# Performance work log

Measured on AMD Instinct MI355X. Metric: run time of the kernel, lower is better.

The kernel has to match this reference:

```python
import jax, jax.numpy as jnp
import numpy as np

B, H, M, D, MID, DV = 128, 8, 196, 128, 64, 128


def setup_inputs() -> dict:
    key0 = jax.random.key(0)
    ks = jax.random.split(key0, 12)
    query = jax.random.normal(ks[0], (B, H, D), dtype=jnp.float32)
    key = jax.random.normal(ks[1], (B, H, M, D), dtype=jnp.float32)
    att_mask = jax.random.randint(ks[2], (B, M), 0, 2).astype(jnp.float32)
    att_mask = att_mask.at[:, 0].set(1.0)  # guarantee each row has >=1 valid slot
    value1 = jax.random.normal(ks[3], (B, H, DV), dtype=jnp.float32)
    value2 = jax.random.normal(ks[4], (B, H, M, DV), dtype=jnp.float32)
    W_basic = jax.random.normal(ks[5], (D, MID), dtype=jnp.float32) * 0.05
    b_basic = jnp.zeros((MID,), dtype=jnp.float32)
    W_spatial = jax.random.normal(ks[6], (MID, 1), dtype=jnp.float32) * 0.05
    b_spatial = jnp.zeros((1,), dtype=jnp.float32)
    W_channel = jax.random.normal(ks[7], (MID, DV), dtype=jnp.float32) * 0.05
    b_channel = jnp.zeros((DV,), dtype=jnp.float32)
    return {
        'query': query, 'key': key, 'att_mask': att_mask,
        'value1': value1, 'value2': value2,
        'W_basic': W_basic, 'b_basic': b_basic,
        'W_spatial': W_spatial, 'b_spatial': b_spatial,
        'W_channel': W_channel, 'b_channel': b_channel,
    }


def reference(query, key, att_mask, value1, value2,
              W_basic, b_basic, W_spatial, b_spatial, W_channel, b_channel):
    # att_map: broadcast elementwise QK product  [B,H,M,D]
    att_map = query[..., None, :] * key
    # attention_basic: Linear + ReLU (Dropout is identity at eval)  [B,H,M,MID]
    h = jax.nn.relu(jnp.einsum('bhmd,de->bhme', att_map, W_basic) + b_basic)
    # masked mean-pool over regions  [B,H,MID]
    mask_ext = att_mask[:, None, :, None]  # [B,1,M,1]
    att_map_pool = jnp.sum(h * mask_ext, axis=-2) / jnp.sum(mask_ext, axis=-2)
    # spatial attention logits  [B,H,M]
    alpha_spatial = (jnp.einsum('bhme,eo->bhmo', h, W_spatial) + b_spatial)[..., 0]
    alpha_spatial = jnp.where(att_mask[:, None, :] == 0, -1e9, alpha_spatial)
    alpha_spatial = jax.nn.softmax(alpha_spatial, axis=-1)
    # weighted sum over regions  [B,H,DV]
    v2 = jnp.einsum('bhm,bhmv->bhv', alpha_spatial, value2)
    # channel gate  [B,H,DV]
    alpha_channel = jax.nn.sigmoid(jnp.einsum('bhe,ev->bhv', att_map_pool, W_channel) + b_channel)
    return value1 * v2 * alpha_channel
```

## Files before the change

kernel.cpp:

```cpp
#include <hip/hip_runtime.h>
#include <cstddef>

#define NBH  1024
#define Mm   196
#define Dd   128
#define MIDe 64
#define DVv  128
#define WQLD 136

typedef __attribute__((ext_vector_type(8))) short bf16x8;
typedef __attribute__((ext_vector_type(4))) float f32x4;

__device__ __forceinline__ short f2bf(float x) {
    union { float f; unsigned u; } v; v.f = x;
    return (short)((v.u + 0x7FFFu + ((v.u >> 16) & 1u)) >> 16);
}

__device__ __forceinline__ void gl_lds16(const void* g, void* l) {
    __builtin_amdgcn_global_load_lds(
        (const __attribute__((address_space(1))) unsigned int*)g,
        (__attribute__((address_space(3))) unsigned int*)l, 16, 0, 0);
}

__global__ __launch_bounds__(256, 2)
void scatt_fused(const float* __restrict__ query,
                 const float* __restrict__ key,
                 const float* __restrict__ att_mask,
                 const float* __restrict__ value1,
                 const float* __restrict__ value2,
                 const float* __restrict__ W_basic,
                 const float* __restrict__ b_basic,
                 const float* __restrict__ W_spatial,
                 const float* __restrict__ b_spatial,
                 const float* __restrict__ W_channel,
                 const float* __restrict__ b_channel,
                 float* __restrict__ out)
{
    __shared__ float4 kb[2][32][16];
    __shared__ short  wqT[MIDe][WQLD];
    __shared__ float  qS[Dd];
    __shared__ float  maskS[Mm];
    __shared__ float  poolS[MIDe];

    const int t    = threadIdx.x;
    const int lane = t & 63;
    const int w    = t >> 6;
    const int ln15 = lane & 15;
    const int q4   = lane >> 4;
    const int bh   = blockIdx.x;
    const int b    = bh >> 3;

    const char*  keyC  = (const char*)(key + (size_t)bh * Mm * Dd);
    const float* val2B = value2   + (size_t)bh * Mm * DVv;
    const float* qB    = query    + (size_t)bh * Dd;
    const float* maskB = att_mask + (size_t)b  * Mm;

    const int cell0 = w * 128 + lane;
    const int cell1 = cell0 + 64;
    const int r0 = cell0 & 15, d40 = cell0 >> 4;
    const int r1 = cell1 & 15, d41 = cell1 >> 4;
    const int so0  = r0 * 512 + d40 * 16;
    const int so1  = r1 * 512 + d41 * 16;
    const int soT0 = (r0 < 4 ? r0 : 3) * 512 + d40 * 16;
    const int soT1 = (r1 < 4 ? r1 : 3) * 512 + d41 * 16;
    const int colOff = w * 32 + 2 * ln15;

    gl_lds16(keyC + so0, (char*)kb + w * 2048);
    gl_lds16(keyC + so1, (char*)kb + w * 2048 + 1024);
    float2 vvA[4], vvB[4];
#pragma unroll
    for (int rr = 0; rr < 4; ++rr)
        vvA[rr] = *(const float2*)(val2B + (size_t)(q4 * 4 + rr) * DVv + colOff);

    if (t < 32) ((float4*)qS)[t] = ((const float4*)qB)[t];
    for (int i = t; i < Mm; i += 256) maskS[i] = maskB[i];
    __syncthreads();
    {
        const int e0 = lane;
        const int d0 = w * 32;
#pragma unroll
        for (int c = 0; c < 4; ++c) {
            short pk[8];
#pragma unroll
            for (int j = 0; j < 8; ++j) {
                const int d = d0 + c * 8 + j;
                pk[j] = f2bf(qS[d] * W_basic[d * MIDe + e0]);
            }
            *(bf16x8*)&wqT[e0][d0 + c * 8] = *(bf16x8*)pk;
        }
    }
    __syncthreads();

    float bbv[4], wspv[4];
#pragma unroll
    for (int nt = 0; nt < 4; ++nt) {
        bbv[nt]  = b_basic[nt * 16 + ln15];
        wspv[nt] = W_spatial[nt * 16 + ln15];
    }
    const float bsp = b_spatial[0];

    float poolAcc[4] = {0.f, 0.f, 0.f, 0.f};
    float m_run = -3.0e38f, l_run = 0.f;
    float2 av = make_float2(0.f, 0.f);

#define TILE_STEP(MT, PAR, VCUR, VNXT, PF)                                   \
    do {                                                                     \
        asm volatile("s_waitcnt vmcnt(4)" ::: "memory");                     \
        __builtin_amdgcn_s_barrier();                                        \
        __builtin_amdgcn_sched_barrier(0);                                   \
        if (PF) {                                                            \
            char* db = (char*)kb + ((PAR) ^ 1) * 8192;                       \
            const char* sb = keyC + (size_t)((MT) + 1) * 8192;               \
            if ((PF) == 1) {                                                 \
                gl_lds16(sb + so0, db + w * 2048);                           \
                gl_lds16(sb + so1, db + w * 2048 + 1024);                    \
            } else {                                                         \
                gl_lds16(sb + soT0, db + w * 2048);                          \
                gl_lds16(sb + soT1, db + w * 2048 + 1024);                   \
            }                                                                \
            __builtin_amdgcn_sched_barrier(0);                               \
            _Pragma("unroll")                                                \
            for (int rr = 0; rr < 4; ++rr) {                                 \
                int vrow = ((MT) + 1) * 16 + q4 * 4 + rr;                    \
                if ((PF) == 2) vrow = vrow < Mm ? vrow : (Mm - 1);           \
                VNXT[rr] =                                                   \
                    *(const float2*)(val2B + (size_t)vrow * DVv + colOff);   \
            }                                                                \
        }                                                                    \
        const char* kbB = (const char*)kb + (PAR) * 8192;                    \
        f32x4 acc[4] = {f32x4{0,0,0,0}, f32x4{0,0,0,0},                      \
                        f32x4{0,0,0,0}, f32x4{0,0,0,0}};                     \
        _Pragma("unroll")                                                    \
        for (int ks = 0; ks < 4; ++ks) {                                     \
            const int d4 = ks * 8 + q4 * 2;                                  \
            const float4 f0 = *(const float4*)(kbB + d4 * 256 + ln15 * 16);  \
            const float4 f1 =                                                \
                *(const float4*)(kbB + d4 * 256 + 256 + ln15 * 16);          \
            const bf16x8 af = { f2bf(f0.x), f2bf(f0.y), f2bf(f0.z),          \
                                f2bf(f0.w), f2bf(f1.x), f2bf(f1.y),          \
                                f2bf(f1.z), f2bf(f1.w) };                    \
            _Pragma("unroll")                                                \
            for (int nt = 0; nt < 4; ++nt) {                                 \
                const bf16x8 bk =                                            \
                    *(const bf16x8*)&wqT[nt * 16 + ln15][ks * 32 + q4 * 8];  \
                acc[nt] = __builtin_amdgcn_mfma_f32_16x16x32_bf16(           \
                              af, bk, acc[nt], 0, 0, 0);                     \
            }                                                                \
        }                                                                    \
        float sR[4];                                                         \
        _Pragma("unroll")                                                    \
        for (int rr = 0; rr < 4; ++rr) {                                     \
            const int m = (MT) * 16 + q4 * 4 + rr;                           \
            const bool valid = m < Mm;                                       \
            const float msk = valid ? maskS[m] : 0.f;                        \
            float srow = 0.f;                                                \
            _Pragma("unroll")                                                \
            for (int nt = 0; nt < 4; ++nt) {                                 \
                float hv = acc[nt][rr] + bbv[nt];                            \
                hv = hv > 0.f ? hv : 0.f;                                    \
                poolAcc[nt] = fmaf(hv, msk, poolAcc[nt]);                    \
                srow = fmaf(hv, wspv[nt], srow);                             \
            }                                                                \
            srow += __shfl_xor(srow, 1, 64);                                 \
            srow += __shfl_xor(srow, 2, 64);                                 \
            srow += __shfl_xor(srow, 4, 64);                                 \
            srow += __shfl_xor(srow, 8, 64);                                 \
            sR[rr] = valid ? (msk == 0.f ? -1.0e9f : srow + bsp) : -3.0e38f; \
        }                                                                    \
        float tm = fmaxf(fmaxf(sR[0], sR[1]), fmaxf(sR[2], sR[3]));          \
        tm = fmaxf(tm, __shfl_xor(tm, 16, 64));                              \
        tm = fmaxf(tm, __shfl_xor(tm, 32, 64));                              \
        const float newm = fmaxf(m_run, tm);                                 \
        const float sc = __expf(m_run - newm);                               \
        m_run = newm;                                                        \
        l_run *= sc; av.x *= sc; av.y *= sc;                                 \
        _Pragma("unroll")                                                    \
        for (int rr = 0; rr < 4; ++rr) {                                     \
            const float p = __expf(sR[rr] - newm);                           \
            l_run += p;                                                      \
            av.x = fmaf(p, VCUR[rr].x, av.x);                                \
            av.y = fmaf(p, VCUR[rr].y, av.y);                                \
        }                                                                    \
    } while (0)

    for (int mtp = 0; mtp < 5; ++mtp) {
        const int mt0 = 2 * mtp;
        TILE_STEP(mt0,     0, vvA, vvB, 1);
        TILE_STEP(mt0 + 1, 1, vvB, vvA, 1);
    }
    TILE_STEP(10, 0, vvA, vvB, 1);
    TILE_STEP(11, 1, vvB, vvA, 2);
    TILE_STEP(12, 0, vvA, vvB, 0);
#undef TILE_STEP

#pragma unroll
    for (int nt = 0; nt < 4; ++nt) {
        poolAcc[nt] += __shfl_xor(poolAcc[nt], 16, 64);
        poolAcc[nt] += __shfl_xor(poolAcc[nt], 32, 64);
    }
    l_run += __shfl_xor(l_run, 16, 64);
    l_run += __shfl_xor(l_run, 32, 64);
    av.x  += __shfl_xor(av.x, 16, 64);
    av.x  += __shfl_xor(av.x, 32, 64);
    av.y  += __shfl_xor(av.y, 16, 64);
    av.y  += __shfl_xor(av.y, 32, 64);

    float cnt = 0.f;
    for (int i = lane; i < Mm; i += 64) cnt += maskS[i];
#pragma unroll
    for (int off = 32; off > 0; off >>= 1) cnt += __shfl_xor(cnt, off, 64);

    if (w == 0 && lane < 16) {
#pragma unroll
        for (int nt = 0; nt < 4; ++nt)
            poolS[nt * 16 + lane] = poolAcc[nt] / cnt;
    }
    __syncthreads();

    const float v2x = av.x / l_run;
    const float v2y = av.y / l_run;

    float a0 = 0.f, a1 = 0.f;
#pragma unroll
    for (int i = 0; i < 16; ++i) {
        const int e = q4 * 16 + i;
        const float pe = poolS[e];
        const float2 wc = *(const float2*)(W_channel + (size_t)e * DVv + colOff);
        a0 = fmaf(pe, wc.x, a0);
        a1 = fmaf(pe, wc.y, a1);
    }
    a0 += __shfl_xor(a0, 16, 64); a0 += __shfl_xor(a0, 32, 64);
    a1 += __shfl_xor(a1, 16, 64); a1 += __shfl_xor(a1, 32, 64);

    if (q4 == 0) {
        const float2 bc = *(const float2*)(b_channel + colOff);
        const float ch0 = 1.f / (1.f + __expf(-(a0 + bc.x)));
        const float ch1 = 1.f / (1.f + __expf(-(a1 + bc.y)));
        const float2 v1 = *(const float2*)(value1 + (size_t)bh * DVv + colOff);
        float2 o;
        o.x = v1.x * v2x * ch0;
        o.y = v1.y * v2y * ch1;
        *(float2*)(out + (size_t)bh * DVv + colOff) = o;
    }
}

extern "C" void kernel_launch(void* const* d_in, const int* in_sizes, int n_in,
                              void* d_out, int out_size, void* d_ws, size_t ws_size,
                              hipStream_t stream) {
    const float* query     = (const float*)d_in[0];
    const float* key       = (const float*)d_in[1];
    const float* att_mask  = (const float*)d_in[2];
    const float* value1    = (const float*)d_in[3];
    const float* value2    = (const float*)d_in[4];
    const float* W_basic   = (const float*)d_in[5];
    const float* b_basic   = (const float*)d_in[6];
    const float* W_spatial = (const float*)d_in[7];
    const float* b_spatial = (const float*)d_in[8];
    const float* W_channel = (const float*)d_in[9];
    const float* b_channel = (const float*)d_in[10];
    float* out = (float*)d_out;

    scatt_fused<<<NBH, 256, 0, stream>>>(query, key, att_mask, value1, value2,
                                         W_basic, b_basic, W_spatial, b_spatial,
                                         W_channel, b_channel, out);
}
```

Measured before the change: 255.1 us.

## Deepen key/value prefetch to triple-buffered LDS with two-tile lookahead

Expands the key LDS buffer from two stages to three and prefetches tiles two steps ahead, with a third register set for value2 rows. Key fragments are now read from LDS and converted to bf16 before the next prefetch is issued, so the barrier protects the buffer being overwritten. The aim is to hide more global-load latency per tile. The cost is more LDS (another 8 KB) and more registers, which may reduce occupancy under the 2-blocks launch bound. The hand-set vmcnt wait counts must stay correct for this to be safe.

```diff
diff --git a/kernel.cpp b/kernel.cpp
--- a/kernel.cpp
+++ b/kernel.cpp
@@ -36,7 +36,7 @@
                  const float* __restrict__ b_channel,
                  float* __restrict__ out)
 {
-    __shared__ float4 kb[2][32][16];
+    __shared__ float4 kb[3][32][16];
     __shared__ short  wqT[MIDe][WQLD];
     __shared__ float  qS[Dd];
     __shared__ float  maskS[Mm];
@@ -67,7 +67,7 @@
 
     gl_lds16(keyC + so0, (char*)kb + w * 2048);
     gl_lds16(keyC + so1, (char*)kb + w * 2048 + 1024);
-    float2 vvA[4], vvB[4];
+    float2 vvA[4], vvB[4], vvC[4];
 #pragma unroll
     for (int rr = 0; rr < 4; ++rr)
         vvA[rr] = *(const float2*)(val2B + (size_t)(q4 * 4 + rr) * DVv + colOff);
@@ -91,6 +91,12 @@
     }
     __syncthreads();
 
+    gl_lds16(keyC + 8192 + so0, (char*)kb + 8192 + w * 2048);
+    gl_lds16(keyC + 8192 + so1, (char*)kb + 8192 + w * 2048 + 1024);
+#pragma unroll
+    for (int rr = 0; rr < 4; ++rr)
+        vvB[rr] = *(const float2*)(val2B + (size_t)(16 + q4 * 4 + rr) * DVv + colOff);
+
     float bbv[4], wspv[4];
 #pragma unroll
     for (int nt = 0; nt < 4; ++nt) {
@@ -103,14 +109,26 @@
     float m_run = -3.0e38f, l_run = 0.f;
     float2 av = make_float2(0.f, 0.f);
 
-#define TILE_STEP(MT, PAR, VCUR, VNXT, PF)                                   \
+#define TILE_STEP(MT, PAR, PNX, VCUR, VN2, PF, WAITASM)                      \
     do {                                                                     \
-        asm volatile("s_waitcnt vmcnt(4)" ::: "memory");                     \
+        asm volatile(WAITASM ::: "memory");                                  \
         __builtin_amdgcn_s_barrier();                                        \
         __builtin_amdgcn_sched_barrier(0);                                   \
+        const char* kbB = (const char*)kb + (PAR) * 8192;                    \
+        bf16x8 af[4];                                                        \
+        _Pragma("unroll")                                                    \
+        for (int ks = 0; ks < 4; ++ks) {                                     \
+            const int d4 = ks * 8 + q4 * 2;                                  \
+            const float4 f0 = *(const float4*)(kbB + d4 * 256 + ln15 * 16);  \
+            const float4 f1 =                                                \
+                *(const float4*)(kbB + d4 * 256 + 256 + ln15 * 16);          \
+            af[ks] = bf16x8{ f2bf(f0.x), f2bf(f0.y), f2bf(f0.z), f2bf(f0.w), \
+                             f2bf(f1.x), f2bf(f1.y), f2bf(f1.z), f2bf(f1.w)};\
+        }                                                                    \
+        __builtin_amdgcn_sched_barrier(0);                                   \
         if (PF) {                                                            \
-            char* db = (char*)kb + ((PAR) ^ 1) * 8192;                       \
-            const char* sb = keyC + (size_t)((MT) + 1) * 8192;               \
+            char* db = (char*)kb + (PNX) * 8192;                             \
+            const char* sb = keyC + (size_t)((MT) + 2) * 8192;               \
             if ((PF) == 1) {                                                 \
                 gl_lds16(sb + so0, db + w * 2048);                           \
                 gl_lds16(sb + so1, db + w * 2048 + 1024);                    \
@@ -118,33 +136,25 @@
                 gl_lds16(sb + soT0, db + w * 2048);                          \
                 gl_lds16(sb + soT1, db + w * 2048 + 1024);                   \
             }                                                                \
-            __builtin_amdgcn_sched_barrier(0);                               \
             _Pragma("unroll")                                                \
             for (int rr = 0; rr < 4; ++rr) {                                 \
-                int vrow = ((MT) + 1) * 16 + q4 * 4 + rr;                    \
+                int vrow = ((MT) + 2) * 16 + q4 * 4 + rr;                    \
                 if ((PF) == 2) vrow = vrow < Mm ? vrow : (Mm - 1);           \
-                VNXT[rr] =                                                   \
+                VN2[rr] =                                                    \
                     *(const float2*)(val2B + (size_t)vrow * DVv + colOff);   \
             }                                                                \
-        }                                                                    \
-        const char* kbB = (const char*)kb + (PAR) * 8192;                    \
+            __builtin_amdgcn_sched_barrier(0);                               \
+        }                                                                    \
         f32x4 acc[4] = {f32x4{0,0,0,0}, f32x4{0,0,0,0},                      \
                         f32x4{0,0,0,0}, f32x4{0,0,0,0}};                     \
         _Pragma("unroll")                                                    \
         for (int ks = 0; ks < 4; ++ks) {                                     \
-            const int d4 = ks * 8 + q4 * 2;                                  \
-            const float4 f0 = *(const float4*)(kbB + d4 * 256 + ln15 * 16);  \
-            const float4 f1 =                                                \
-                *(const float4*)(kbB + d4 * 256 + 256 + ln15 * 16);          \
-            const bf16x8 af = { f2bf(f0.x), f2bf(f0.y), f2bf(f0.z),          \
-                                f2bf(f0.w), f2bf(f1.x), f2bf(f1.y),          \
-                                f2bf(f1.z), f2bf(f1.w) };                    \
             _Pragma("unroll")                                                \
             for (int nt = 0; nt < 4; ++nt) {                                 \
                 const bf16x8 bk =                                            \
                     *(const bf16x8*)&wqT[nt * 16 + ln15][ks * 32 + q4 * 8];  \
                 acc[nt] = __builtin_amdgcn_mfma_f32_16x16x32_bf16(           \
-                              af, bk, acc[nt], 0, 0, 0);                     \
+                              af[ks], bk, acc[nt], 0, 0, 0);                 \
             }                                                                \
         }                                                                    \
         float sR[4];                                                         \
@@ -183,14 +193,16 @@
         }                                                                    \
     } while (0)
 
-    for (int mtp = 0; mtp < 5; ++mtp) {
-        const int mt0 = 2 * mtp;
-        TILE_STEP(mt0,     0, vvA, vvB, 1);
-        TILE_STEP(mt0 + 1, 1, vvB, vvA, 1);
-    }
-    TILE_STEP(10, 0, vvA, vvB, 1);
-    TILE_STEP(11, 1, vvB, vvA, 2);
-    TILE_STEP(12, 0, vvA, vvB, 0);
+    for (int g = 0; g < 3; ++g) {
+        const int t0 = g * 3;
+        TILE_STEP(t0,     0, 2, vvA, vvC, 1, "s_waitcnt vmcnt(10)");
+        TILE_STEP(t0 + 1, 1, 0, vvB, vvA, 1, "s_waitcnt vmcnt(10)");
+        TILE_STEP(t0 + 2, 2, 1, vvC, vvB, 1, "s_waitcnt vmcnt(10)");
+    }
+    TILE_STEP(9,  0, 2, vvA, vvC, 1, "s_waitcnt vmcnt(10)");
+    TILE_STEP(10, 1, 0, vvB, vvA, 2, "s_waitcnt vmcnt(10)");
+    TILE_STEP(11, 2, 1, vvC, vvB, 0, "s_waitcnt vmcnt(10)");
+    TILE_STEP(12, 0, 2, vvA, vvC, 0, "s_waitcnt vmcnt(4)");
 #undef TILE_STEP
 
 #pragma unroll
```

Result: faster. 247.5 us (-3.0%).
